# Performance work log

Measured on AMD Instinct MI355X. Metric: run time of the kernel, lower is better.

Reference implementation:

```python
import jax, jax.numpy as jnp
import numpy as np
import math

DIMS, HEAD = 1024, 16
HD = DIMS // HEAD          # 64
B, CTX = 4, 1024
MAX_ITER, THRESH = 3, 0.5  # temp=1.0 -> q temperature scaling branch is skipped (as in torch)
LOG10_21 = math.log10(1.0 + 4000.0 / 200.0)


def _freq_angles(c):
    # compute_freqs_base: 0.2*(10**linspace(0, log10(21), d/2) - 1), custom_freqs = 36000/220 * base
    d2 = HD // 2
    mel = 10.0 ** jnp.linspace(0.0, LOG10_21, d2) - 1.0
    freqs = (36000.0 / 220.0) * (200.0 * mel / 1000.0)        # [d2]
    t = jnp.arange(c, dtype=jnp.float32)
    return t[:, None] * freqs[None, :]                          # [c, d2]


def _rope(x, ang):
    # lucidrains rotary_embedding_torch convention: interleaved pairs (x0,x1),(x2,x3),...
    x1, x2 = x[..., 0::2], x[..., 1::2]
    cos, sin = jnp.cos(ang), jnp.sin(ang)
    out = jnp.stack([x1 * cos - x2 * sin, x1 * sin + x2 * cos], axis=-1)
    return out.reshape(x.shape)


def _rms(x, w):
    eps = jnp.finfo(x.dtype).eps  # torch nn.RMSNorm eps=None default
    return x * jax.lax.rsqrt(jnp.mean(jnp.square(x), -1, keepdims=True) + eps) * w


def _sdpa(q, k, v):
    # mask is always None in this module's forward -> non-causal SDPA
    s = jnp.einsum('bhqd,bhkd->bhqk', q, k) / math.sqrt(q.shape[-1])
    return jnp.einsum('bhqk,bhkd->bhqd', jax.nn.softmax(s, -1), v)


def _focus(x, xa, P):
    # x: [b, cq, D] queries, xa: [b, ck, D] keys/values. In our configs cq == ck == eff_span.
    b, cq, D = x.shape
    ck = xa.shape[1]
    q = _rms(x, P['wq_norm']) @ P['Wq'] + P['bq']
    q = q.reshape(b, cq, HEAD, HD).transpose(0, 2, 1, 3)                 # b h c d
    kv = _rms(xa, P['wkv_norm']) @ P['Wkv'] + P['bkv']
    kv = kv.reshape(b, ck, 2, HEAD, HD).transpose(2, 0, 3, 1, 4)         # kv b h c d
    k, v = kv[0], kv[1]
    q = _rope(q, _freq_angles(cq))
    k = _rope(k, _freq_angles(ck))

    e = min(cq, ck)  # static; equals cq in all call sites here
    curq, kc, vc = q, k[:, :, :e], v[:, :, :e]
    prev = jnp.zeros_like(q)
    attn_out = jnp.zeros_like(q)
    done = jnp.asarray(False)
    for it in range(MAX_ITER):
        # torch: q/k/v re-projected from current state EVERY iteration (k,v compound)
        qp = curq[:, :, :e] @ P['Wlq'] + P['blq']
        kp = kc @ P['Wlk'] + P['blk']
        vp = vc @ P['Wlv'] + P['blv']
        attn = _sdpa(_rms(qp, P['wln']), _rms(kp, P['wln']), vp)         # == iter_out since e == cq
        diff = jnp.mean(jnp.abs(attn - prev))
        stop = (diff < THRESH) & (it > 0) & (~done)
        attn_out = jnp.where(done, attn_out, attn)  # on the break iteration attn_out = iter_out
        done = done | stop
        curq = jnp.where(done, curq, curq + attn)
        prev = jnp.where(done, prev, attn)
        kc = jnp.where(done, kc, kp)
        vc = jnp.where(done, vc, vp)
    return attn_out.transpose(0, 2, 1, 3).reshape(b, cq, D)             # b c (h d)


def _slide(x, P):
    # win_size = head_dim; only the first win_size keys of each span are ever used
    b, ctx, D = x.shape
    w = HD
    off = w // HEAD                       # span_len - win_size
    nwin = ctx // w                       # ctx chosen as a multiple of w
    starts = jnp.maximum(jnp.arange(nwin) * w - off, 0)
    kidx = starts[:, None] + jnp.arange(w)[None, :]                      # [nwin, w]
    qwin = x.reshape(b, nwin, w, D).transpose(1, 0, 2, 3)                # [nwin, b, w, D]
    kwin = x[:, kidx, :].transpose(1, 0, 2, 3)                           # [nwin, b, w, D]
    outw = jax.vmap(lambda xq, xk: _focus(xq, xk, P))(qwin, kwin)
    return outw.transpose(1, 0, 2, 3).reshape(b, ctx, D)


def _forward(x, xa, P):
    xw = _slide(x, P)
    xaw = _slide(xa, P)
    out = _focus(xw, xaw, P)
    return out @ P['Wo'] + P['bo']        # Dropout(0.01) is identity in eval


def setup_inputs() -> dict:
    key = jax.random.key(0)
    ks = jax.random.split(key, 8)
    s = 0.02
    f32 = jnp.float32
    return {
        'x': jax.random.normal(ks[0], (B, CTX, DIMS), f32),
        'xa': jax.random.normal(ks[1], (B, CTX, DIMS), f32),
        'wq_norm': jnp.ones((DIMS,), f32),
        'Wq': jax.random.normal(ks[2], (DIMS, DIMS), f32) * s,
        'bq': jnp.zeros((DIMS,), f32),
        'wkv_norm': jnp.ones((DIMS,), f32),
        'Wkv': jax.random.normal(ks[3], (DIMS, 2 * DIMS), f32) * s,
        'bkv': jnp.zeros((2 * DIMS,), f32),
        'wln': jnp.ones((HD,), f32),
        'Wlq': jax.random.normal(ks[4], (HD, HD), f32) * s,
        'blq': jnp.zeros((HD,), f32),
        'Wlk': jax.random.normal(ks[5], (HD, HD), f32) * s,
        'blk': jnp.zeros((HD,), f32),
        'Wlv': jax.random.normal(ks[6], (HD, HD), f32) * s,
        'blv': jnp.zeros((HD,), f32),
        'Wo': jax.random.normal(ks[7], (DIMS, DIMS), f32) * s,
        'bo': jnp.zeros((DIMS,), f32),
    }


def reference(x, xa, wq_norm, Wq, bq, wkv_norm, Wkv, bkv, wln, Wlq, blq, Wlk, blk, Wlv, blv, Wo, bo):
    P = dict(wq_norm=wq_norm, Wq=Wq, bq=bq, wkv_norm=wkv_norm, Wkv=Wkv, bkv=bkv, wln=wln,
             Wlq=Wlq, blq=blq, Wlk=Wlk, blk=blk, Wlv=Wlv, blv=blv, Wo=Wo, bo=bo)
    return _forward(x, xa, P)
```

## Files before the change

### kernel.cpp

```cpp
#include <hip/hip_runtime.h>
#include <math.h>

#define TPB 256

static __device__ __forceinline__ float4 mk4(float a, float b, float c, float d) {
  float4 r; r.x = a; r.y = b; r.z = c; r.w = d; return r;
}

static __device__ __forceinline__ float4 ld4s(const float* buf, int row, int ch) {
  return *(const float4*)&buf[(row << 6) + (((ch ^ (row >> 2)) & 15) << 2)];
}
static __device__ __forceinline__ void st4s(float* buf, int row, int ch, float4 v) {
  *(float4*)&buf[(row << 6) + (((ch ^ (row >> 2)) & 15) << 2)] = v;
}

__global__ __launch_bounds__(TPB) void k_tables(float* __restrict__ cosb,
                                                float* __restrict__ sinb) {
  int gid = blockIdx.x * TPB + threadIdx.x;
  if (gid >= 1024 * 32) return;
  int t = gid >> 5, j = gid & 31;
  const double Ld = 1.3222192947339193;
  float Lf = (float)Ld;
  float mlog;
  if (j == 31) {
    mlog = Lf;
  } else {
    float stepf = (float)((double)j / 31.0);
    mlog = (float)((double)Lf * (double)stepf);
  }
  float p = (float)pow(10.0, (double)mlog);
  float mel = p - 1.0f;
  float t2 = (200.0f * mel) / 1000.0f;
  float freq = 163.63636363636363f * t2;
  float ang = (float)t * freq;
  double a = (double)ang;
  cosb[gid] = (float)cos(a);
  sinb[gid] = (float)sin(a);
}

__global__ __launch_bounds__(TPB) void k_rowinv(const float* __restrict__ X,
                                                float* __restrict__ inv) {
  __shared__ float red[4];
  int row = blockIdx.x;
  int tid = threadIdx.x;
  float4 v = *(const float4*)(X + (size_t)row * 1024 + tid * 4);
  float ss = v.x * v.x + v.y * v.y + v.z * v.z + v.w * v.w;
#pragma unroll
  for (int m = 1; m < 64; m <<= 1) ss += __shfl_xor(ss, m);
  if ((tid & 63) == 0) red[tid >> 6] = ss;
  __syncthreads();
  if (tid == 0) {
    float s = ((red[0] + red[1]) + (red[2] + red[3]));
    float mm = s * (1.0f / 1024.0f) + 1.1920928955078125e-7f;
    inv[row] = (float)(1.0 / sqrt((double)mm));
  }
}

template <int BM, int BN>
__global__ __launch_bounds__(TPB) void k_gemm(
    const float* __restrict__ X, const float* __restrict__ inv,
    const float* __restrict__ wn, const float* __restrict__ W,
    const float* __restrict__ bias, float* __restrict__ o0,
    float* __restrict__ o1, int N, int mode) {
  constexpr int JW = BN / 64;
  constexpr int RH = BM / 64;
  constexpr int TPR = 256 / BM;
  __shared__ float As[16][BM + 4];
  int tid = threadIdx.x;
  int bx = blockIdx.x, by = blockIdx.y;
  int tx = tid & 15, ty = tid >> 4;
  float c[4 * RH][4 * JW];
#pragma unroll
  for (int i = 0; i < 4 * RH; ++i)
#pragma unroll
    for (int j = 0; j < 4 * JW; ++j) c[i][j] = 0.0f;

  int arow = tid / TPR;
  int kqb[RH];
#pragma unroll
  for (int u = 0; u < RH; ++u) kqb[u] = ((tid % TPR) * RH + u) * 4;
  float sA = 1.0f;
  if (inv) sA = inv[by * BM + arow];
  const float* Xrow = X + (size_t)(by * BM + arow) * 1024;
  const float* Wb = W + bx * BN + tx * 4;

  float4 areg[RH];
#pragma unroll
  for (int u = 0; u < RH; ++u)
    areg[u] = *(const float4*)(Xrow + kqb[u]);

  for (int k0 = 0; k0 < 1024; k0 += 16) {
#pragma unroll
    for (int u = 0; u < RH; ++u) {
      int kq = kqb[u];
      float4 a4 = areg[u];
      if (wn) {
        float4 w4 = *(const float4*)(wn + k0 + kq);
        a4.x *= w4.x; a4.y *= w4.y; a4.z *= w4.z; a4.w *= w4.w;
      }
      a4.x *= sA; a4.y *= sA; a4.z *= sA; a4.w *= sA;
      As[kq + 0][arow] = a4.x;
      As[kq + 1][arow] = a4.y;
      As[kq + 2][arow] = a4.z;
      As[kq + 3][arow] = a4.w;
    }
    __syncthreads();
    if (k0 + 16 < 1024) {
#pragma unroll
      for (int u = 0; u < RH; ++u)
        areg[u] = *(const float4*)(Xrow + k0 + 16 + kqb[u]);
    }
#pragma unroll
    for (int kk = 0; kk < 16; ++kk) {
      float av[4 * RH];
      float4 a0 = *(const float4*)&As[kk][ty * 4];
      av[0] = a0.x; av[1] = a0.y; av[2] = a0.z; av[3] = a0.w;
      if (RH == 2) {
        float4 a1 = *(const float4*)&As[kk][64 + ty * 4];
        av[4] = a1.x; av[5] = a1.y; av[6] = a1.z; av[7] = a1.w;
      }
      const float* wrow = Wb + (size_t)(k0 + kk) * N;
      float4 b0 = *(const float4*)(wrow);
      float bv[4 * JW];
      bv[0] = b0.x; bv[1] = b0.y; bv[2] = b0.z; bv[3] = b0.w;
      if (JW == 2) {
        float4 b1 = *(const float4*)(wrow + 64);
        bv[4] = b1.x; bv[5] = b1.y; bv[6] = b1.z; bv[7] = b1.w;
      }
#pragma unroll
      for (int i = 0; i < 4 * RH; ++i)
#pragma unroll
        for (int j = 0; j < 4 * JW; ++j) c[i][j] += av[i] * bv[j];
    }
    __syncthreads();
  }

#pragma unroll
  for (int jh = 0; jh < JW; ++jh) {
    int colbase = bx * BN + jh * 64 + tx * 4;
    float4 bb = {0.f, 0.f, 0.f, 0.f};
    if (bias) bb = *(const float4*)(bias + colbase);
#pragma unroll
    for (int ih = 0; ih < RH; ++ih) {
#pragma unroll
      for (int i2 = 0; i2 < 4; ++i2) {
        int row = by * BM + ih * 64 + ty * 4 + i2;
        int ci = ih * 4 + i2;
        float4 o;
        o.x = c[ci][jh * 4 + 0] + bb.x;
        o.y = c[ci][jh * 4 + 1] + bb.y;
        o.z = c[ci][jh * 4 + 2] + bb.z;
        o.w = c[ci][jh * 4 + 3] + bb.w;
        if (mode == 0) {
          *(float4*)(o0 + (size_t)row * N + colbase) = o;
        } else {
          int b = row >> 10, t = row & 1023;
          float* dst = o0;
          int cc = colbase;
          if (mode == 2 && colbase >= 1024) { dst = o1; cc = colbase - 1024; }
          int ch = cc >> 6, d = cc & 63;
          *(float4*)(dst + ((size_t)((b * 16 + ch) * 1024 + t)) * 64 + d) = o;
        }
      }
    }
  }
}

__global__ __launch_bounds__(TPB) void k_rope(float* __restrict__ A, int mask,
                                              const float* __restrict__ cosb,
                                              const float* __restrict__ sinb) {
  int gid = blockIdx.x * TPB + threadIdx.x;
  int j = gid & 31;
  int row = gid >> 5;
  int t = row & 1023;
  int aidx = ((t & mask) << 5) + j;
  float cc = cosb[aidx], sn = sinb[aidx];
  size_t base = (size_t)row * 64;
  float x1 = A[base + 2 * j], x2 = A[base + 2 * j + 1];
  A[base + 2 * j] = x1 * cc - x2 * sn;
  A[base + 2 * j + 1] = x1 * sn + x2 * cc;
}

__global__ __launch_bounds__(TPB) void k_proj(
    const float* __restrict__ curq, float* __restrict__ kc,
    float* __restrict__ vc, float* __restrict__ qph, float* __restrict__ kph,
    const float* __restrict__ Wlq, const float* __restrict__ blq,
    const float* __restrict__ Wlk, const float* __restrict__ blk,
    const float* __restrict__ Wlv, const float* __restrict__ blv,
    const float* __restrict__ wln, int CQ, const int* __restrict__ flags) {
  int RT = CQ >> 4;
  int bid = blockIdx.x;
  int rt = bid % RT;
  int rest = bid / RT;
  int h = rest & 15; rest >>= 4;
  int b = rest & 3;
  int win = rest >> 2;
  if (flags && flags[win]) return;
  __shared__ float qs[16][68], ksm[16][68], vsm[16][68];
  __shared__ float Wqs[4096], Wks[4096], Wvs[4096];
  int tid = threadIdx.x;
#pragma unroll
  for (int i = 0; i < 4; ++i) {
    int f4 = (i * 256 + tid) * 4;
    *(float4*)&Wqs[f4] = *(const float4*)(Wlq + f4);
    *(float4*)&Wks[f4] = *(const float4*)(Wlk + f4);
    *(float4*)&Wvs[f4] = *(const float4*)(Wlv + f4);
  }
  int lr = tid >> 4, c4 = (tid & 15) * 4;
  int bh = b * 16 + h;
  size_t rowbase = (size_t)bh * 1024 + (size_t)win * CQ + rt * 16;
  size_t g = (rowbase + lr) * 64 + c4;
  *(float4*)&qs[lr][c4] = *(const float4*)(curq + g);
  *(float4*)&ksm[lr][c4] = *(const float4*)(kc + g);
  *(float4*)&vsm[lr][c4] = *(const float4*)(vc + g);
  __syncthreads();
  int r = tid >> 4, cg = tid & 15;
  const float eps = 1.1920928955078125e-7f;
  float4 wl4 = *(const float4*)(wln + cg * 4);
  size_t orow = (rowbase + r) * 64 + cg * 4;
  float4 acc;
  float ssum, rms;
  acc = *(const float4*)(blq + cg * 4);
#pragma unroll 8
  for (int k = 0; k < 64; ++k) {
    float xv = qs[r][k];
    float4 w4 = *(const float4*)&Wqs[k * 64 + cg * 4];
    acc.x += xv * w4.x; acc.y += xv * w4.y;
    acc.z += xv * w4.z; acc.w += xv * w4.w;
  }
  ssum = acc.x * acc.x + acc.y * acc.y + acc.z * acc.z + acc.w * acc.w;
#pragma unroll
  for (int m = 1; m < 16; m <<= 1) ssum += __shfl_xor(ssum, m);
  rms = (float)(1.0 / sqrt((double)(ssum * 0.015625f + eps)));
  {
    float4 o;
    o.x = acc.x * rms * wl4.x; o.y = acc.y * rms * wl4.y;
    o.z = acc.z * rms * wl4.z; o.w = acc.w * rms * wl4.w;
    *(float4*)(qph + orow) = o;
  }
  acc = *(const float4*)(blk + cg * 4);
#pragma unroll 8
  for (int k = 0; k < 64; ++k) {
    float xv = ksm[r][k];
    float4 w4 = *(const float4*)&Wks[k * 64 + cg * 4];
    acc.x += xv * w4.x; acc.y += xv * w4.y;
    acc.z += xv * w4.z; acc.w += xv * w4.w;
  }
  *(float4*)(kc + orow) = acc;
  ssum = acc.x * acc.x + acc.y * acc.y + acc.z * acc.z + acc.w * acc.w;
#pragma unroll
  for (int m = 1; m < 16; m <<= 1) ssum += __shfl_xor(ssum, m);
  rms = (float)(1.0 / sqrt((double)(ssum * 0.015625f + eps)));
  {
    float4 o;
    o.x = acc.x * rms * wl4.x; o.y = acc.y * rms * wl4.y;
    o.z = acc.z * rms * wl4.z; o.w = acc.w * rms * wl4.w;
    *(float4*)(kph + orow) = o;
  }
  acc = *(const float4*)(blv + cg * 4);
#pragma unroll 8
  for (int k = 0; k < 64; ++k) {
    float xv = vsm[r][k];
    float4 w4 = *(const float4*)&Wvs[k * 64 + cg * 4];
    acc.x += xv * w4.x; acc.y += xv * w4.y;
    acc.z += xv * w4.z; acc.w += xv * w4.w;
  }
  *(float4*)(vc + orow) = acc;
}

static __device__ __forceinline__ void slide_proj_one(
    float* src, float* rawdst, float* ndst, const float* __restrict__ W,
    const float* __restrict__ bias, float4 wl4, int tx, int ty) {
  const float eps = 1.1920928955078125e-7f;
  float4 bb = *(const float4*)(bias + tx * 4);
  float4 acc[4];
#pragma unroll
  for (int i = 0; i < 4; ++i) acc[i] = bb;
#pragma unroll 2
  for (int k4 = 0; k4 < 16; ++k4) {
    const float* w = W + (k4 * 4) * 64 + tx * 4;
    float4 w0 = *(const float4*)(w);
    float4 w1 = *(const float4*)(w + 64);
    float4 w2 = *(const float4*)(w + 128);
    float4 w3 = *(const float4*)(w + 192);
#pragma unroll
    for (int i = 0; i < 4; ++i) {
      float4 a4 = ld4s(src, ty * 4 + i, k4);
      acc[i].x += a4.x * w0.x; acc[i].y += a4.x * w0.y;
      acc[i].z += a4.x * w0.z; acc[i].w += a4.x * w0.w;
      acc[i].x += a4.y * w1.x; acc[i].y += a4.y * w1.y;
      acc[i].z += a4.y * w1.z; acc[i].w += a4.y * w1.w;
      acc[i].x += a4.z * w2.x; acc[i].y += a4.z * w2.y;
      acc[i].z += a4.z * w2.z; acc[i].w += a4.z * w2.w;
      acc[i].x += a4.w * w3.x; acc[i].y += a4.w * w3.y;
      acc[i].z += a4.w * w3.z; acc[i].w += a4.w * w3.w;
    }
  }
#pragma unroll
  for (int i = 0; i < 4; ++i) {
    int row = ty * 4 + i;
    if (rawdst) st4s(rawdst, row, tx, acc[i]);
    if (ndst) {
      float ssum = acc[i].x * acc[i].x + acc[i].y * acc[i].y +
                   acc[i].z * acc[i].z + acc[i].w * acc[i].w;
#pragma unroll
      for (int mm = 1; mm < 16; mm <<= 1) ssum += __shfl_xor(ssum, mm);
      float rms = (float)(1.0 / sqrt((double)(ssum * 0.015625f + eps)));
      st4s(ndst, row, tx, mk4(acc[i].x * rms * wl4.x, acc[i].y * rms * wl4.y,
                              acc[i].z * rms * wl4.z, acc[i].w * rms * wl4.w));
    }
  }
}

__global__ __launch_bounds__(TPB) void k_slide(
    const float* __restrict__ Qg, const float* __restrict__ Kg,
    const float* __restrict__ Vg, float* __restrict__ curqg,
    float* __restrict__ kcg, float* __restrict__ vcg, float* __restrict__ outb,
    float* __restrict__ diffp, const int* __restrict__ flags,
    const float* __restrict__ cosb, const float* __restrict__ sinb,
    const float* __restrict__ Wlq, const float* __restrict__ blq,
    const float* __restrict__ Wlk, const float* __restrict__ blk,
    const float* __restrict__ Wlv, const float* __restrict__ blv,
    const float* __restrict__ wln, int mode) {
  int bid = blockIdx.x;
  int win = bid & 15, bh = bid >> 4;
  int h = bh & 15, b = bh >> 4;
  if (mode == 2 && flags[win]) return;
  __shared__ float sX[4096], sKc[4096], sVc[4096], sQp[4096], sKp[4096];
  int tid = threadIdx.x;
  int tx = tid & 15, ty = tid >> 4;
  size_t bh1024 = (size_t)bh * 1024;
  int t0 = win * 64;
  const float SCL = 0.18033688011112042f;

  if (mode == 0) {
    int sw = (win == 0) ? 0 : win * 64 - 4;
#pragma unroll
    for (int u = 0; u < 4; ++u) {
      int f4 = u * 256 + tid;
      int row = f4 >> 4, ch = f4 & 15;
      int aidx = (row << 5) + ch * 2;
      float c0 = cosb[aidx], s0 = sinb[aidx];
      float c1 = cosb[aidx + 1], s1 = sinb[aidx + 1];
      float4 q = *(const float4*)(Qg + (bh1024 + t0 + row) * 64 + ch * 4);
      st4s(sX, row, ch, mk4(q.x * c0 - q.y * s0, q.x * s0 + q.y * c0,
                            q.z * c1 - q.w * s1, q.z * s1 + q.w * c1));
      float4 k = *(const float4*)(Kg + (bh1024 + sw + row) * 64 + ch * 4);
      st4s(sKc, row, ch, mk4(k.x * c0 - k.y * s0, k.x * s0 + k.y * c0,
                             k.z * c1 - k.w * s1, k.z * s1 + k.w * c1));
      st4s(sVc, row, ch,
           *(const float4*)(Vg + (bh1024 + sw + row) * 64 + ch * 4));
    }
  } else {
#pragma unroll
    for (int u = 0; u < 4; ++u) {
      int f4 = u * 256 + tid;
      int row = f4 >> 4, ch = f4 & 15;
      size_t g = (bh1024 + t0 + row) * 64 + ch * 4;
      st4s(sX, row, ch, *(const float4*)(curqg + g));
      st4s(sKc, row, ch, *(const float4*)(kcg + g));
      st4s(sVc, row, ch, *(const float4*)(vcg + g));
    }
  }
  float4 wl4 = *(const float4*)(wln + tx * 4);
  float4 prev4[4];
  int niter = (mode == 0) ? 2 : 1;
  for (int it = 0; it < niter; ++it) {
    __syncthreads();
    slide_proj_one(sX, nullptr, sQp, Wlq, blq, wl4, tx, ty);
    slide_proj_one(sKc, sKc, sKp, Wlk, blk, wl4, tx, ty);
    slide_proj_one(sVc, sVc, nullptr, Wlv, blv, wl4, tx, ty);
    __syncthreads();
    float s4[4][4];
#pragma unroll
    for (int i = 0; i < 4; ++i)
      s4[i][0] = s4[i][1] = s4[i][2] = s4[i][3] = 0.0f;
#pragma unroll 4
    for (int d4 = 0; d4 < 16; ++d4) {
      float4 kv[4];
#pragma unroll
      for (int j = 0; j < 4; ++j) kv[j] = ld4s(sKp, tx * 4 + j, d4);
#pragma unroll
      for (int i = 0; i < 4; ++i) {
        float4 q4 = ld4s(sQp, ty * 4 + i, d4);
#pragma unroll
        for (int j = 0; j < 4; ++j) {
          s4[i][j] += q4.x * kv[j].x;
          s4[i][j] += q4.y * kv[j].y;
          s4[i][j] += q4.z * kv[j].z;
          s4[i][j] += q4.w * kv[j].w;
        }
      }
    }
    float lrow[4];
#pragma unroll
    for (int i = 0; i < 4; ++i) {
      s4[i][0] *= SCL; s4[i][1] *= SCL; s4[i][2] *= SCL; s4[i][3] *= SCL;
      float r0 = fmaxf(fmaxf(s4[i][0], s4[i][1]), fmaxf(s4[i][2], s4[i][3]));
#pragma unroll
      for (int mm = 1; mm < 16; mm <<= 1) r0 = fmaxf(r0, __shfl_xor(r0, mm));
      float rs = 0.0f;
#pragma unroll
      for (int j = 0; j < 4; ++j) {
        float pv = exp2f(s4[i][j] - r0);
        s4[i][j] = pv;
        rs += pv;
      }
#pragma unroll
      for (int mm = 1; mm < 16; mm <<= 1) rs += __shfl_xor(rs, mm);
      lrow[i] = rs;
    }
#pragma unroll
    for (int i = 0; i < 4; ++i)
      st4s(sQp, ty * 4 + i, tx, mk4(s4[i][0], s4[i][1], s4[i][2], s4[i][3]));
    float4 av[4];
#pragma unroll
    for (int i = 0; i < 4; ++i) av[i] = mk4(0.f, 0.f, 0.f, 0.f);
#pragma unroll 4
    for (int k4 = 0; k4 < 16; ++k4) {
      float4 v4[4];
#pragma unroll
      for (int kk = 0; kk < 4; ++kk) v4[kk] = ld4s(sVc, k4 * 4 + kk, tx);
#pragma unroll
      for (int i = 0; i < 4; ++i) {
        float4 p4 = ld4s(sQp, ty * 4 + i, k4);
        av[i].x += p4.x * v4[0].x; av[i].y += p4.x * v4[0].y;
        av[i].z += p4.x * v4[0].z; av[i].w += p4.x * v4[0].w;
        av[i].x += p4.y * v4[1].x; av[i].y += p4.y * v4[1].y;
        av[i].z += p4.y * v4[1].z; av[i].w += p4.y * v4[1].w;
        av[i].x += p4.z * v4[2].x; av[i].y += p4.z * v4[2].y;
        av[i].z += p4.z * v4[2].z; av[i].w += p4.z * v4[2].w;
        av[i].x += p4.w * v4[3].x; av[i].y += p4.w * v4[3].y;
        av[i].z += p4.w * v4[3].z; av[i].w += p4.w * v4[3].w;
      }
    }
#pragma unroll
    for (int i = 0; i < 4; ++i) {
      av[i].x /= lrow[i]; av[i].y /= lrow[i];
      av[i].z /= lrow[i]; av[i].w /= lrow[i];
    }
    if (mode == 0 && it == 0) {
#pragma unroll
      for (int i = 0; i < 4; ++i) {
        prev4[i] = av[i];
        int row = ty * 4 + i;
        float4 cq = ld4s(sX, row, tx);
        cq.x += av[i].x; cq.y += av[i].y; cq.z += av[i].z; cq.w += av[i].w;
        st4s(sX, row, tx, cq);
      }
    } else if (mode == 0) {
      float ds = 0.0f;
#pragma unroll
      for (int i = 0; i < 4; ++i) {
        int row = ty * 4 + i;
        ds += fabsf(av[i].x - prev4[i].x) + fabsf(av[i].y - prev4[i].y) +
              fabsf(av[i].z - prev4[i].z) + fabsf(av[i].w - prev4[i].w);
        float4 cq = ld4s(sX, row, tx);
        cq.x += av[i].x; cq.y += av[i].y; cq.z += av[i].z; cq.w += av[i].w;
        st4s(sX, row, tx, cq);
        size_t g = (bh1024 + t0 + row) * 64 + tx * 4;
        *(float4*)(curqg + g) = cq;
        *(float4*)(kcg + g) = ld4s(sKc, row, tx);
        *(float4*)(vcg + g) = ld4s(sVc, row, tx);
        size_t obase = ((size_t)b * 1024 + t0 + row) * 1024 + h * 64 + tx * 4;
        *(float4*)(outb + obase) = av[i];
      }
      __syncthreads();
      float* red = sKp;
      red[tid] = ds;
      __syncthreads();
      for (int s2 = 128; s2 > 0; s2 >>= 1) {
        if (tid < s2) red[tid] += red[tid + s2];
        __syncthreads();
      }
      if (tid == 0) diffp[bid] = red[0];
    } else {
#pragma unroll
      for (int i = 0; i < 4; ++i) {
        int row = ty * 4 + i;
        size_t obase = ((size_t)b * 1024 + t0 + row) * 1024 + h * 64 + tx * 4;
        *(float4*)(outb + obase) = av[i];
      }
    }
  }
}

__global__ __launch_bounds__(TPB) void k_attn7(
    const float* __restrict__ qph, const float* __restrict__ kph,
    const float* __restrict__ vbuf, float* __restrict__ curq,
    float* __restrict__ prevb, float* __restrict__ outb,
    float* __restrict__ diffp, const int* __restrict__ flags, int NQT, int nt,
    int mode) {
  int bid = blockIdx.x;
  int qt = bid % NQT;
  int bh = bid / NQT;
  int h = bh & 15, b = bh >> 4;
  if (mode == 2 && flags[0]) return;
  __shared__ float sK[4096];
  __shared__ float sV[4096];
  __shared__ float sP[8192];
  int tid = threadIdx.x;
  int tx = tid & 15, ty = tid >> 4;
  size_t bh1024 = (size_t)bh * 1024;
  int q0 = qt * 128;
  const float* Qb = qph + (bh1024 + q0 + ty * 8) * 64;

  float m[8], l[8], acc[8][4];
#pragma unroll
  for (int i = 0; i < 8; ++i) {
    m[i] = -INFINITY; l[i] = 0.0f;
    acc[i][0] = acc[i][1] = acc[i][2] = acc[i][3] = 0.0f;
  }
  const float SCL = 0.18033688011112042f;

  float4 kreg[4], vreg[4];
#pragma unroll
  for (int u = 0; u < 4; ++u) {
    int f4 = u * 256 + tid;
    int row = f4 >> 4, ch = f4 & 15;
    kreg[u] = *(const float4*)(kph + (bh1024 + row) * 64 + ch * 4);
    vreg[u] = *(const float4*)(vbuf + (bh1024 + row) * 64 + ch * 4);
  }

  for (int kt = 0; kt < nt; ++kt) {
#pragma unroll
    for (int u = 0; u < 4; ++u) {
      int f4 = u * 256 + tid;
      int row = f4 >> 4, ch = f4 & 15;
      st4s(sK, row, ch, kreg[u]);
      st4s(sV, row, ch, vreg[u]);
    }
    __syncthreads();
    if (kt + 1 < nt) {
      int k0n = (kt + 1) * 64;
#pragma unroll
      for (int u = 0; u < 4; ++u) {
        int f4 = u * 256 + tid;
        int row = f4 >> 4, ch = f4 & 15;
        kreg[u] = *(const float4*)(kph + (bh1024 + k0n + row) * 64 + ch * 4);
        vreg[u] = *(const float4*)(vbuf + (bh1024 + k0n + row) * 64 + ch * 4);
      }
    }
    float s[8][4];
#pragma unroll
    for (int i = 0; i < 8; ++i)
      s[i][0] = s[i][1] = s[i][2] = s[i][3] = 0.0f;
#pragma unroll 4
    for (int d4 = 0; d4 < 16; ++d4) {
      float4 kv[4];
#pragma unroll
      for (int j = 0; j < 4; ++j) kv[j] = ld4s(sK, tx * 4 + j, d4);
#pragma unroll
      for (int i = 0; i < 8; ++i) {
        float4 q4 = *(const float4*)(Qb + i * 64 + d4 * 4);
#pragma unroll
        for (int j = 0; j < 4; ++j) {
          s[i][j] += q4.x * kv[j].x;
          s[i][j] += q4.y * kv[j].y;
          s[i][j] += q4.z * kv[j].z;
          s[i][j] += q4.w * kv[j].w;
        }
      }
    }
#pragma unroll
    for (int i = 0; i < 8; ++i) {
      s[i][0] *= SCL; s[i][1] *= SCL; s[i][2] *= SCL; s[i][3] *= SCL;
      float r0 = fmaxf(fmaxf(s[i][0], s[i][1]), fmaxf(s[i][2], s[i][3]));
#pragma unroll
      for (int mm = 1; mm < 16; mm <<= 1) r0 = fmaxf(r0, __shfl_xor(r0, mm));
      float mnew = fmaxf(m[i], r0);
      float sc = exp2f(m[i] - mnew);
      float rs = 0.0f;
#pragma unroll
      for (int j = 0; j < 4; ++j) {
        float pv = exp2f(s[i][j] - mnew);
        s[i][j] = pv;
        rs += pv;
      }
#pragma unroll
      for (int mm = 1; mm < 16; mm <<= 1) rs += __shfl_xor(rs, mm);
      l[i] = l[i] * sc + rs;
      m[i] = mnew;
      acc[i][0] *= sc; acc[i][1] *= sc; acc[i][2] *= sc; acc[i][3] *= sc;
    }
#pragma unroll
    for (int i = 0; i < 8; ++i) {
      int q = ty * 8 + i;
      *(float4*)&sP[(q << 6) + (((tx ^ (q >> 3)) & 15) << 2)] =
          mk4(s[i][0], s[i][1], s[i][2], s[i][3]);
    }
#pragma unroll 4
    for (int k4 = 0; k4 < 16; ++k4) {
      float4 v4[4];
#pragma unroll
      for (int kk = 0; kk < 4; ++kk) v4[kk] = ld4s(sV, k4 * 4 + kk, tx);
#pragma unroll
      for (int i = 0; i < 8; ++i) {
        int q = ty * 8 + i;
        float4 p4 = *(const float4*)&sP[(q << 6) +
                                        (((k4 ^ (q >> 3)) & 15) << 2)];
        acc[i][0] += p4.x * v4[0].x; acc[i][1] += p4.x * v4[0].y;
        acc[i][2] += p4.x * v4[0].z; acc[i][3] += p4.x * v4[0].w;
        acc[i][0] += p4.y * v4[1].x; acc[i][1] += p4.y * v4[1].y;
        acc[i][2] += p4.y * v4[1].z; acc[i][3] += p4.y * v4[1].w;
        acc[i][0] += p4.z * v4[2].x; acc[i][1] += p4.z * v4[2].y;
        acc[i][2] += p4.z * v4[2].z; acc[i][3] += p4.z * v4[2].w;
        acc[i][0] += p4.w * v4[3].x; acc[i][1] += p4.w * v4[3].y;
        acc[i][2] += p4.w * v4[3].z; acc[i][3] += p4.w * v4[3].w;
      }
    }
    __syncthreads();
  }
  float ds = 0.0f;
#pragma unroll
  for (int i = 0; i < 8; ++i) {
    int t = q0 + ty * 8 + i;
    float4 att;
    att.x = acc[i][0] / l[i];
    att.y = acc[i][1] / l[i];
    att.z = acc[i][2] / l[i];
    att.w = acc[i][3] / l[i];
    size_t base = (bh1024 + t) * 64 + tx * 4;
    size_t obase = ((size_t)b * 1024 + t) * 1024 + h * 64 + tx * 4;
    if (mode == 0) {
      *(float4*)(prevb + base) = att;
      float4 cq = *(const float4*)(curq + base);
      cq.x += att.x; cq.y += att.y; cq.z += att.z; cq.w += att.w;
      *(float4*)(curq + base) = cq;
    } else if (mode == 1) {
      float4 pv = *(const float4*)(prevb + base);
      ds += fabsf(att.x - pv.x) + fabsf(att.y - pv.y) +
            fabsf(att.z - pv.z) + fabsf(att.w - pv.w);
      float4 cq = *(const float4*)(curq + base);
      cq.x += att.x; cq.y += att.y; cq.z += att.z; cq.w += att.w;
      *(float4*)(curq + base) = cq;
      *(float4*)(outb + obase) = att;
    } else {
      *(float4*)(outb + obase) = att;
    }
  }
  if (mode == 1) {
    __syncthreads();
    float* red = sP;
    red[tid] = ds;
    __syncthreads();
    for (int s2 = 128; s2 > 0; s2 >>= 1) {
      if (tid < s2) red[tid] += red[tid + s2];
      __syncthreads();
    }
    if (tid == 0) diffp[bid] = red[0];
  }
}

__global__ __launch_bounds__(64) void k_finalize(const float* __restrict__ diffp,
                                                 int* __restrict__ flags,
                                                 int nwin, int nper,
                                                 float count) {
  int w = threadIdx.x;
  if (w < nwin) {
    float s = 0.0f;
    for (int i = 0; i < nper; ++i) s += diffp[w + i * nwin];
    flags[w] = (s / count < 0.5f) ? 1 : 0;
  }
}

extern "C" void kernel_launch(void* const* d_in, const int* in_sizes, int n_in,
                              void* d_out, int out_size, void* d_ws,
                              size_t ws_size, hipStream_t stream) {
  const float* x = (const float*)d_in[0];
  const float* xa = (const float*)d_in[1];
  const float* wqn = (const float*)d_in[2];
  const float* Wq = (const float*)d_in[3];
  const float* bq = (const float*)d_in[4];
  const float* wkvn = (const float*)d_in[5];
  const float* Wkv = (const float*)d_in[6];
  const float* bkv = (const float*)d_in[7];
  const float* wln = (const float*)d_in[8];
  const float* Wlq = (const float*)d_in[9];
  const float* blq = (const float*)d_in[10];
  const float* Wlk = (const float*)d_in[11];
  const float* blk = (const float*)d_in[12];
  const float* Wlv = (const float*)d_in[13];
  const float* blv = (const float*)d_in[14];
  const float* Wo = (const float*)d_in[15];
  const float* bo = (const float*)d_in[16];

  float* ws = (float*)d_ws;
  const size_t SLOT = (size_t)4 * 16 * 1024 * 64;
  float* xw = ws;
  float* xaw = ws + SLOT;
  float* Q = ws + 2 * SLOT;
  float* K = ws + 3 * SLOT;
  float* V = ws + 4 * SLOT;
  float* kc = ws + 5 * SLOT;
  float* vc = ws + 6 * SLOT;
  float* prev = ws + 7 * SLOT;
  float* qph = ws + 8 * SLOT;
  float* kph = ws + 9 * SLOT;
  float* misc = ws + 10 * SLOT;
  float* inv = misc;
  float* cosb = misc + 8192;
  float* sinb = cosb + 32768;
  float* diffp = sinb + 32768;
  int* flags = (int*)(diffp + 4096);

  k_tables<<<128, TPB, 0, stream>>>(cosb, sinb);

  for (int sl = 0; sl < 2; ++sl) {
    const float* Xin = sl ? xa : x;
    float* Xout = sl ? xaw : xw;
    k_rowinv<<<4096, TPB, 0, stream>>>(Xin, inv);
    k_gemm<64, 128><<<dim3(8, 64), TPB, 0, stream>>>(Xin, inv, wqn, Wq, bq, Q, nullptr, 1024, 1);
    k_gemm<128, 128><<<dim3(16, 32), TPB, 0, stream>>>(Xin, inv, wkvn, Wkv, bkv, K, V, 2048, 2);
    k_slide<<<1024, TPB, 0, stream>>>(Q, K, V, Q, kc, vc, Xout, diffp, nullptr,
                                      cosb, sinb, Wlq, blq, Wlk, blk, Wlv, blv,
                                      wln, 0);
    k_finalize<<<1, 64, 0, stream>>>(diffp, flags, 16, 64, 262144.0f);
    k_slide<<<1024, TPB, 0, stream>>>(Q, K, V, Q, kc, vc, Xout, diffp, flags,
                                      cosb, sinb, Wlq, blq, Wlk, blk, Wlv, blv,
                                      wln, 2);
  }

  k_rowinv<<<4096, TPB, 0, stream>>>(xw, inv);
  k_gemm<64, 128><<<dim3(8, 64), TPB, 0, stream>>>(xw, inv, wqn, Wq, bq, Q, nullptr, 1024, 1);
  k_rowinv<<<4096, TPB, 0, stream>>>(xaw, inv);
  k_gemm<128, 128><<<dim3(16, 32), TPB, 0, stream>>>(xaw, inv, wkvn, Wkv, bkv, K, V, 2048, 2);
  k_rope<<<8192, TPB, 0, stream>>>(Q, 1023, cosb, sinb);
  k_rope<<<8192, TPB, 0, stream>>>(K, 1023, cosb, sinb);
  float* fout = xw;
  k_proj<<<4096, TPB, 0, stream>>>(Q, K, V, qph, kph, Wlq, blq, Wlk, blk, Wlv, blv, wln, 1024, nullptr);
  k_attn7<<<512, TPB, 0, stream>>>(qph, kph, V, Q, prev, fout, diffp, nullptr, 8, 16, 0);
  k_proj<<<4096, TPB, 0, stream>>>(Q, K, V, qph, kph, Wlq, blq, Wlk, blk, Wlv, blv, wln, 1024, nullptr);
  k_attn7<<<512, TPB, 0, stream>>>(qph, kph, V, Q, prev, fout, diffp, nullptr, 8, 16, 1);
  k_finalize<<<1, 64, 0, stream>>>(diffp, flags, 1, 512, 4194304.0f);
  k_proj<<<4096, TPB, 0, stream>>>(Q, K, V, qph, kph, Wlq, blq, Wlk, blk, Wlv, blv, wln, 1024, flags);
  k_attn7<<<512, TPB, 0, stream>>>(qph, kph, V, Q, prev, fout, diffp, flags, 8, 16, 2);

  k_gemm<64, 128><<<dim3(8, 64), TPB, 0, stream>>>(fout, nullptr, nullptr, Wo, bo, (float*)d_out, nullptr, 1024, 0);
}
```

Measured before the change: 2.775 ms.

## Shrink attention P scratch to quarter tiles and drop register K/V prefetch

The attention kernel now stages the probability tile in four 16-key quarters through a 128x16 shared buffer instead of the full 128x64 tile. This cuts shared memory per block from 64KB to 40KB. It also removes the register double-buffering of the next K/V tile and loads straight from global into shared memory, which lowers register pressure. The goal is more resident blocks per CU. The cost is losing the overlap of global loads with compute, and correctness now depends on wave-synchronous LDS access within a 16-lane row group, since there is no barrier between the quarter writes and reads.

New measurement: 5.585 ms. 2.01x slower.

```diff
diff --git a/kernel.cpp b/kernel.cpp
--- a/kernel.cpp
+++ b/kernel.cpp
@@ -485,7 +485,7 @@
   }
 }
 
-__global__ __launch_bounds__(TPB) void k_attn7(
+__global__ __launch_bounds__(TPB) void k_attn8(
     const float* __restrict__ qph, const float* __restrict__ kph,
     const float* __restrict__ vbuf, float* __restrict__ curq,
     float* __restrict__ prevb, float* __restrict__ outb,
@@ -498,7 +498,7 @@
   if (mode == 2 && flags[0]) return;
   __shared__ float sK[4096];
   __shared__ float sV[4096];
-  __shared__ float sP[8192];
+  __shared__ float sP[2048];
   int tid = threadIdx.x;
   int tx = tid & 15, ty = tid >> 4;
   size_t bh1024 = (size_t)bh * 1024;
@@ -512,35 +512,21 @@
     acc[i][0] = acc[i][1] = acc[i][2] = acc[i][3] = 0.0f;
   }
   const float SCL = 0.18033688011112042f;
-
-  float4 kreg[4], vreg[4];
-#pragma unroll
-  for (int u = 0; u < 4; ++u) {
-    int f4 = u * 256 + tid;
-    int row = f4 >> 4, ch = f4 & 15;
-    kreg[u] = *(const float4*)(kph + (bh1024 + row) * 64 + ch * 4);
-    vreg[u] = *(const float4*)(vbuf + (bh1024 + row) * 64 + ch * 4);
-  }
+  int myqtr = tx >> 2;
+  int mych = (tx & 3) * 4;
 
   for (int kt = 0; kt < nt; ++kt) {
+    int k0 = kt * 64;
 #pragma unroll
     for (int u = 0; u < 4; ++u) {
       int f4 = u * 256 + tid;
       int row = f4 >> 4, ch = f4 & 15;
-      st4s(sK, row, ch, kreg[u]);
-      st4s(sV, row, ch, vreg[u]);
+      st4s(sK, row, ch,
+           *(const float4*)(kph + (bh1024 + k0 + row) * 64 + ch * 4));
+      st4s(sV, row, ch,
+           *(const float4*)(vbuf + (bh1024 + k0 + row) * 64 + ch * 4));
     }
     __syncthreads();
-    if (kt + 1 < nt) {
-      int k0n = (kt + 1) * 64;
-#pragma unroll
-      for (int u = 0; u < 4; ++u) {
-        int f4 = u * 256 + tid;
-        int row = f4 >> 4, ch = f4 & 15;
-        kreg[u] = *(const float4*)(kph + (bh1024 + k0n + row) * 64 + ch * 4);
-        vreg[u] = *(const float4*)(vbuf + (bh1024 + k0n + row) * 64 + ch * 4);
-      }
-    }
     float s[8][4];
 #pragma unroll
     for (int i = 0; i < 8; ++i)
@@ -584,29 +570,33 @@
       acc[i][0] *= sc; acc[i][1] *= sc; acc[i][2] *= sc; acc[i][3] *= sc;
     }
 #pragma unroll
-    for (int i = 0; i < 8; ++i) {
-      int q = ty * 8 + i;
-      *(float4*)&sP[(q << 6) + (((tx ^ (q >> 3)) & 15) << 2)] =
-          mk4(s[i][0], s[i][1], s[i][2], s[i][3]);
-    }
-#pragma unroll 4
-    for (int k4 = 0; k4 < 16; ++k4) {
-      float4 v4[4];
-#pragma unroll
-      for (int kk = 0; kk < 4; ++kk) v4[kk] = ld4s(sV, k4 * 4 + kk, tx);
-#pragma unroll
-      for (int i = 0; i < 8; ++i) {
-        int q = ty * 8 + i;
-        float4 p4 = *(const float4*)&sP[(q << 6) +
-                                        (((k4 ^ (q >> 3)) & 15) << 2)];
-        acc[i][0] += p4.x * v4[0].x; acc[i][1] += p4.x * v4[0].y;
-        acc[i][2] += p4.x * v4[0].z; acc[i][3] += p4.x * v4[0].w;
-        acc[i][0] += p4.y * v4[1].x; acc[i][1] += p4.y * v4[1].y;
-        acc[i][2] += p4.y * v4[1].z; acc[i][3] += p4.y * v4[1].w;
-        acc[i][0] += p4.z * v4[2].x; acc[i][1] += p4.z * v4[2].y;
-        acc[i][2] += p4.z * v4[2].z; acc[i][3] += p4.z * v4[2].w;
-        acc[i][0] += p4.w * v4[3].x; acc[i][1] += p4.w * v4[3].y;
-        acc[i][2] += p4.w * v4[3].z; acc[i][3] += p4.w * v4[3].w;
+    for (int qtr = 0; qtr < 4; ++qtr) {
+      if (myqtr == qtr) {
+#pragma unroll
+        for (int i = 0; i < 8; ++i) {
+          int q = ty * 8 + i;
+          *(float4*)&sP[(q << 4) + mych] = mk4(s[i][0], s[i][1], s[i][2], s[i][3]);
+        }
+      }
+#pragma unroll
+      for (int k4 = 0; k4 < 4; ++k4) {
+        float4 v4[4];
+#pragma unroll
+        for (int kk = 0; kk < 4; ++kk)
+          v4[kk] = ld4s(sV, qtr * 16 + k4 * 4 + kk, tx);
+#pragma unroll
+        for (int i = 0; i < 8; ++i) {
+          int q = ty * 8 + i;
+          float4 p4 = *(const float4*)&sP[(q << 4) + k4 * 4];
+          acc[i][0] += p4.x * v4[0].x; acc[i][1] += p4.x * v4[0].y;
+          acc[i][2] += p4.x * v4[0].z; acc[i][3] += p4.x * v4[0].w;
+          acc[i][0] += p4.y * v4[1].x; acc[i][1] += p4.y * v4[1].y;
+          acc[i][2] += p4.y * v4[1].z; acc[i][3] += p4.y * v4[1].w;
+          acc[i][0] += p4.z * v4[2].x; acc[i][1] += p4.z * v4[2].y;
+          acc[i][2] += p4.z * v4[2].z; acc[i][3] += p4.z * v4[2].w;
+          acc[i][0] += p4.w * v4[3].x; acc[i][1] += p4.w * v4[3].y;
+          acc[i][2] += p4.w * v4[3].z; acc[i][3] += p4.w * v4[3].w;
+        }
       }
     }
     __syncthreads();
@@ -641,7 +631,7 @@
   }
   if (mode == 1) {
     __syncthreads();
-    float* red = sP;
+    float* red = sK;
     red[tid] = ds;
     __syncthreads();
     for (int s2 = 128; s2 > 0; s2 >>= 1) {
@@ -729,12 +719,12 @@
   k_rope<<<8192, TPB, 0, stream>>>(K, 1023, cosb, sinb);
   float* fout = xw;
   k_proj<<<4096, TPB, 0, stream>>>(Q, K, V, qph, kph, Wlq, blq, Wlk, blk, Wlv, blv, wln, 1024, nullptr);
-  k_attn7<<<512, TPB, 0, stream>>>(qph, kph, V, Q, prev, fout, diffp, nullptr, 8, 16, 0);
+  k_attn8<<<512, TPB, 0, stream>>>(qph, kph, V, Q, prev, fout, diffp, nullptr, 8, 16, 0);
   k_proj<<<4096, TPB, 0, stream>>>(Q, K, V, qph, kph, Wlq, blq, Wlk, blk, Wlv, blv, wln, 1024, nullptr);
-  k_attn7<<<512, TPB, 0, stream>>>(qph, kph, V, Q, prev, fout, diffp, nullptr, 8, 16, 1);
+  k_attn8<<<512, TPB, 0, stream>>>(qph, kph, V, Q, prev, fout, diffp, nullptr, 8, 16, 1);
   k_finalize<<<1, 64, 0, stream>>>(diffp, flags, 1, 512, 4194304.0f);
   k_proj<<<4096, TPB, 0, stream>>>(Q, K, V, qph, kph, Wlq, blq, Wlk, blk, Wlv, blv, wln, 1024, flags);
-  k_attn7<<<512, TPB, 0, stream>>>(qph, kph, V, Q, prev, fout, diffp, flags, 8, 16, 2);
+  k_attn8<<<512, TPB, 0, stream>>>(qph, kph, V, Q, prev, fout, diffp, flags, 8, 16, 2);
 
   k_gemm<64, 128><<<dim3(8, 64), TPB, 0, stream>>>(fout, nullptr, nullptr, Wo, bo, (float*)d_out, nullptr, 1024, 0);
 }
```
